# Optimization experiments

Hardware: AMD Instinct MI355X
Metric: run time of the kernel (lower is better)

## Reference

```python
import jax, jax.numpy as jnp
import numpy as np

B, T, N, SD, D, HYP, EMB = 128, 256, 8, 200, 64, 64, 32

def _ln(x, g, b, eps=1e-5):
    mu = jnp.mean(x, -1, keepdims=True)
    v = jnp.mean((x - mu) ** 2, -1, keepdims=True)
    return (x - mu) * jax.lax.rsqrt(v + eps) * g + b

def setup_inputs():
    key = jax.random.key(0)
    ks = iter(jax.random.split(key, 64))
    def p(shape, scale=0.05):
        return (jax.random.normal(next(ks), shape) * scale).astype(jnp.float32)
    n, sd, d, hyp, emb = N, SD, D, HYP, EMB
    return dict(
        qvals=p((B, T, n), 1.0), states=p((B, T, sd), 1.0), hidden_state=p((B, T, n, d), 1.0),
        enc_w1=p((sd, d)), enc_b1=p((d,)), enc_w2=p((d, d)), enc_b2=p((d,)),
        wq=p((d, d)), bq=p((d,)), wk=p((d, d)), bk=p((d,)), wv=p((d, d)), bv=p((d,)),
        wo=p((d, d)), bo=p((d,)),
        ln1_g=jnp.ones((d,), jnp.float32), ln1_b=jnp.zeros((d,), jnp.float32),
        ffn_w1=p((d, d)), ffn_b1=p((d,)), ffn_w2=p((d, d)), ffn_b2=p((d,)),
        ln2_g=jnp.ones((d,), jnp.float32), ln2_b=jnp.zeros((d,), jnp.float32),
        fc2ni_w=p((n, d, n - 1)), fc2ni_b=p((n, n - 1)),
        norm_g=jnp.ones((n - 1,), jnp.float32), norm_b=jnp.zeros((n - 1,), jnp.float32),
        w1a=p((2 * d, hyp)), b1a=p((hyp,)), w1b=p((hyp, n * emb)), b1b=p((n * emb,)),
        hb1w=p((2 * d, emb)), hb1b=p((emb,)),
        w2a=p((2 * d, hyp)), b2a=p((hyp,)), w2b=p((hyp, emb)), b2b=p((emb,)),
        hb2w1=p((2 * d, emb)), hb2b1=p((emb,)), hb2w2=p((emb, 1)), hb2b2=p((1,)))

def reference(qvals, states, hidden_state, enc_w1, enc_b1, enc_w2, enc_b2,
              wq, bq, wk, bk, wv, bv, wo, bo, ln1_g, ln1_b,
              ffn_w1, ffn_b1, ffn_w2, ffn_b2, ln2_g, ln2_b,
              fc2ni_w, fc2ni_b, norm_g, norm_b,
              w1a, b1a, w1b, b1b, hb1w, hb1b,
              w2a, b2a, w2b, b2b, hb2w1, hb2b1, hb2w2, hb2b2):
    sg = jax.lax.stop_gradient
    b, t, n = qvals.shape
    bt = b * t
    d = hidden_state.shape[-1]
    emb = hb1w.shape[1]
    # Encoder_s: relu(fc1) then tanh(fc2(e)+e)
    s = states.reshape(bt, -1)
    e = jax.nn.relu(s @ enc_w1 + enc_b1)
    enc = jnp.tanh(e @ enc_w2 + enc_b2 + e)                       # (bt, 64)
    # concat detached agent hiddens with detached state embedding -> (bt, n+1, 64)
    h = jnp.concatenate([sg(hidden_state.reshape(bt, n, d)), sg(enc)[:, None, :]], axis=1)
    # transformer block (single-head self-attention + FFN, post-LN)
    q = h @ wq + bq; k = h @ wk + bk; v = h @ wv + bv
    att = jax.nn.softmax(jnp.einsum('bid,bjd->bij', q, k) / jnp.sqrt(jnp.float32(d)), axis=-1)
    h2 = _ln(h + (att @ v) @ wo + bo, ln1_g, ln1_b)
    h3 = _ln(h2 + jax.nn.relu(h2 @ ffn_w1 + ffn_b1) @ ffn_w2 + ffn_b2, ln2_g, ln2_b)
    h_trans = h3[:, :n]                                           # (bt, n, 64)
    ens = jnp.concatenate([enc, sg(h_trans).mean(1)], axis=-1)    # (bt, 128)
    # per-agent fc2_Ni -> LayerNorm -> sigmoid, vectorized over agents
    ni = jnp.einsum('xnd,nde->xne', h_trans, fc2ni_w) + fc2ni_b   # (bt, n, n-1)
    ni = jax.nn.sigmoid(_ln(ni, norm_g, norm_b))
    # insert 1.0 at the diagonal (agent i keeps its own q with weight 1)
    rows = jnp.arange(n)[:, None]; cols = jnp.arange(n)[None, :]
    gidx = jnp.clip(cols - (cols > rows).astype(jnp.int32), 0, n - 2)  # (n, n)
    gathered = jnp.take_along_axis(ni, jnp.broadcast_to(gidx, (bt, n, n)), axis=-1)
    nfull = jnp.where(cols == rows, jnp.float32(1.0), gathered)   # (bt, n, n)
    N_nn = nfull.reshape(b, t, n, n)
    q_ni = (qvals[:, :, None, :] * N_nn).sum(-1).reshape(bt, 1, n)
    # hypernetwork mixing (QMIX)
    ens_d = sg(ens)
    w1 = jnp.abs(jax.nn.relu(ens_d @ w1a + b1a) @ w1b + b1b).reshape(bt, n, emb)
    b1 = (ens_d @ hb1w + hb1b).reshape(bt, 1, emb)
    w2 = jnp.abs(jax.nn.relu(ens @ w2a + b2a) @ w2b + b2b).reshape(bt, emb, 1)
    b2 = (jax.nn.relu(ens @ hb2w1 + hb2b1) @ hb2w2 + hb2b2).reshape(bt, 1, 1)
    hidden = jax.nn.elu(q_ni @ w1 + b1)
    y = (hidden @ w2 + b2).reshape(b, t, 1)
    eye_mask = jnp.broadcast_to(jnp.eye(n, dtype=bool), (b, t, n, n))
    return y, N_nn, eye_mask
```

## Files before the change

kernel.cpp:

```cpp
#include <hip/hip_runtime.h>
#include <hip/hip_bf16.h>

typedef __bf16 bf16x8 __attribute__((ext_vector_type(8)));
typedef __bf16 bf16x4 __attribute__((ext_vector_type(4)));
typedef float f32x4 __attribute__((ext_vector_type(4)));

#define ROWSG 32768
#define RB 7
#define NBLK 4682
#define HPAD 72
#define NN_OFF ((size_t)ROWSG)
#define EYE_OFF ((size_t)ROWSG + (size_t)ROWSG*64)

#define OFF_EW1   0
#define OFF_EW2   14336
#define OFF_WQ    18432
#define OFF_WK    22528
#define OFF_WV    26624
#define OFF_WO    30720
#define OFF_F1    34816
#define OFF_F2    38912
#define OFF_W1A   43008
#define OFF_W1B   51200
#define OFF_HB1W  67584
#define OFF_W2A   71680
#define OFF_W2B   79872
#define OFF_HB2W1 81920
#define OFF_NI    86016
#define WS_TOTAL  94208

__device__ __align__(16) __bf16 g_ws[WS_TOTAL];

#define MFMA16(a,b,c) __builtin_amdgcn_mfma_f32_16x16x32_bf16(a,b,c,0,0,0)

struct TP { const float* src[15]; };

__global__ __launch_bounds__(256) void wtrans(TP tp) {
    const int gid = blockIdx.x * 256 + threadIdx.x;
    if (gid >= WS_TOTAL) return;
    if (gid >= OFF_NI) {
        const int loc = gid - OFF_NI;
        const int nmat = loc >> 10, rem = loc & 1023, e = rem >> 6, k = rem & 63;
        float v = (e < 7) ? tp.src[14][nmat * 448 + k * 7 + e] : 0.f;
        g_ws[gid] = (__bf16)v;
        return;
    }
    const int OFFS[14] = {OFF_EW1, OFF_EW2, OFF_WQ, OFF_WK, OFF_WV, OFF_WO, OFF_F1,
                          OFF_F2, OFF_W1A, OFF_W1B, OFF_HB1W, OFF_W2A, OFF_W2B, OFF_HB2W1};
    const int KPS[14]  = {224, 64, 64, 64, 64, 64, 64, 64, 128, 64, 128, 128, 64, 128};
    const int KRS[14]  = {200, 64, 64, 64, 64, 64, 64, 64, 128, 64, 128, 128, 64, 128};
    const int NS[14]   = {64, 64, 64, 64, 64, 64, 64, 64, 64, 256, 32, 64, 32, 32};
    int m = 0;
#pragma unroll
    for (int i = 1; i < 14; ++i) if (gid >= OFFS[i]) m = i;
    const int loc = gid - OFFS[m];
    const int Kp = KPS[m];
    const int n = loc / Kp;
    const int k = loc - n * Kp;
    float v = 0.f;
    if (k < KRS[m]) v = tp.src[m][(size_t)k * NS[m] + n];
    g_ws[gid] = (__bf16)v;
}

struct MainP {
    const float *qvals, *states, *hid, *eb1, *eb2, *bq, *bk, *bv, *bo,
        *l1g, *l1b, *fb1, *fb2, *l2g, *l2b, *niw, *nib, *ng, *nb,
        *b1a, *b1b, *hb1b, *b2a, *b2b, *hb2b1, *hw2, *hb2b2;
    float* out;
};

__device__ __forceinline__ void proj_ln4(const __bf16* A, const __bf16* WT,
                                         const float* bias, const float* g, const float* bb,
                                         __bf16* H, int w, int quad, int l15) {
    const int mt = w;
    f32x4 acc0 = {0,0,0,0}, acc1 = {0,0,0,0}, acc2 = {0,0,0,0}, acc3 = {0,0,0,0};
#pragma unroll
    for (int ks = 0; ks < 2; ++ks) {
        const int kk = ks * 32 + quad * 8;
        const bf16x8 af = *(const bf16x8*)(A + (mt * 16 + l15) * HPAD + kk);
        acc0 = MFMA16(af, *(const bf16x8*)(WT + (size_t)(0 * 16 + l15) * 64 + kk), acc0);
        acc1 = MFMA16(af, *(const bf16x8*)(WT + (size_t)(1 * 16 + l15) * 64 + kk), acc1);
        acc2 = MFMA16(af, *(const bf16x8*)(WT + (size_t)(2 * 16 + l15) * 64 + kk), acc2);
        acc3 = MFMA16(af, *(const bf16x8*)(WT + (size_t)(3 * 16 + l15) * 64 + kk), acc3);
    }
    float v[4][4], g4[4], b4[4];
#pragma unroll
    for (int nt = 0; nt < 4; ++nt) {
        const int col = nt * 16 + l15;
        const float bo = bias[col];
        g4[nt] = g[col]; b4[nt] = bb[col];
        const f32x4 a = (nt == 0) ? acc0 : (nt == 1) ? acc1 : (nt == 2) ? acc2 : acc3;
#pragma unroll
        for (int r = 0; r < 4; ++r)
            v[nt][r] = a[r] + bo + (float)H[(mt * 16 + quad * 4 + r) * HPAD + col];
    }
#pragma unroll
    for (int r = 0; r < 4; ++r) {
        float s  = v[0][r] + v[1][r] + v[2][r] + v[3][r];
        float s2 = v[0][r]*v[0][r] + v[1][r]*v[1][r] + v[2][r]*v[2][r] + v[3][r]*v[3][r];
#pragma unroll
        for (int off = 1; off < 16; off <<= 1) {
            s  += __shfl_xor(s,  off, 64);
            s2 += __shfl_xor(s2, off, 64);
        }
        const float mu  = s * 0.015625f;
        const float var = s2 * 0.015625f - mu * mu;
        const float rs  = rsqrtf(var + 1e-5f);
#pragma unroll
        for (int nt = 0; nt < 4; ++nt)
            H[(mt * 16 + quad * 4 + r) * HPAD + nt * 16 + l15] =
                (__bf16)((v[nt][r] - mu) * rs * g4[nt] + b4[nt]);
    }
}

__global__ __launch_bounds__(256) void mixer_main(MainP p) {
    __shared__ __align__(16) __bf16 Hb[64 * HPAD];
    __shared__ __align__(16) __bf16 Qb[64 * HPAD];
    __shared__ __align__(16) __bf16 Kb[64 * HPAD];
    __shared__ __align__(16) __bf16 EbU[16 * HPAD];
    __shared__ __align__(16) float  attU[7 * 90];
    __shared__ float  qniL[56];

    __bf16* Sb   = Qb;
    __bf16* W1bS = Qb;
    float*  B1f  = (float*)(Qb + 1792);
    float*  W2f  = (float*)(Qb + 2240);
    float*  T3f  = (float*)(Qb + 2688);
    __bf16* Tb2  = Qb + 3136;
    float*  sNiP = (float*)(Qb + 3136);
    __bf16* ensB = Kb;

    const int blk = blockIdx.x;
    const int bt0 = blk * RB;
    const int t = threadIdx.x;
    const int w = t >> 6, lane = t & 63, quad = lane >> 4, l15 = lane & 15;
    const __bf16* ws = g_ws;

#pragma unroll
    for (int it = 0; it < 4; ++it) {
        const int u = it * 256 + t;
        if (u < 896) {
            const int x = u >> 7, rem = u & 127, n = rem >> 4, d4 = (rem & 15) * 4;
            const int bt = bt0 + x;
            const size_t btc = (bt < ROWSG) ? bt : (ROWSG - 1);
            const float4 v4 = *(const float4*)(p.hid + (btc * 512 + n * 64 + d4));
            bf16x4 o; o[0] = (__bf16)v4.x; o[1] = (__bf16)v4.y; o[2] = (__bf16)v4.z; o[3] = (__bf16)v4.w;
            *(bf16x4*)(Hb + (x * 9 + n) * HPAD + d4) = o;
        }
    }
#pragma unroll
    for (int it = 0; it < 2; ++it) {
        const int u = it * 256 + t;
        if (u < 350) {
            const int xr = u / 50, c4 = u - xr * 50;
            const int bt = bt0 + xr;
            const size_t btc = (bt < ROWSG) ? bt : (ROWSG - 1);
            const float4 v4 = *(const float4*)(p.states + btc * 200 + c4 * 4);
            bf16x4 o; o[0] = (__bf16)v4.x; o[1] = (__bf16)v4.y; o[2] = (__bf16)v4.z; o[3] = (__bf16)v4.w;
            *(bf16x4*)(Sb + xr * 224 + c4 * 4) = o;
        }
    }
    if (t < 168) { const int xr = t / 24, c = t - xr * 24; Sb[xr * 224 + 200 + c] = (__bf16)0.0f; }
    __syncthreads();

    float e4[4];
    {
        const int n0 = w * 16;
        const int srow = (l15 < RB) ? l15 : (RB - 1);
        f32x4 acc = {0, 0, 0, 0};
        for (int ks = 0; ks < 7; ++ks) {
            const int kk = ks * 32 + quad * 8;
            const bf16x8 af = *(const bf16x8*)(Sb + srow * 224 + kk);
            const bf16x8 bf = *(const bf16x8*)(ws + OFF_EW1 + (size_t)(n0 + l15) * 224 + kk);
            acc = MFMA16(af, bf, acc);
        }
        const float b1 = p.eb1[n0 + l15];
#pragma unroll
        for (int r = 0; r < 4; ++r) {
            const float ev = fmaxf(acc[r] + b1, 0.f);
            e4[r] = ev;
            EbU[(quad * 4 + r) * HPAD + n0 + l15] = (__bf16)ev;
        }
    }
    __syncthreads();

    {
        const int n0 = w * 16;
        f32x4 acc = {0, 0, 0, 0};
#pragma unroll
        for (int ks = 0; ks < 2; ++ks) {
            const int kk = ks * 32 + quad * 8;
            const bf16x8 af = *(const bf16x8*)(EbU + l15 * HPAD + kk);
            const bf16x8 bf = *(const bf16x8*)(ws + OFF_EW2 + (size_t)(n0 + l15) * 64 + kk);
            acc = MFMA16(af, bf, acc);
        }
        const float b2 = p.eb2[n0 + l15];
#pragma unroll
        for (int r = 0; r < 4; ++r) {
            const int xr = quad * 4 + r;
            if (xr < RB) {
                const float ev = tanhf(acc[r] + e4[r] + b2);
                Hb[(xr * 9 + 8) * HPAD + n0 + l15] = (__bf16)ev;
                EbU[(8 + xr) * HPAD + n0 + l15] = (__bf16)ev;
            }
        }
    }
    __syncthreads();

    for (int it = 0; it < 8; ++it) {
        const int j = w + 4 * it;
        const int mat = j >> 4, r16 = j & 15, mt = r16 >> 2, nt = r16 & 3;
        const __bf16* wt = ws + (mat == 0 ? OFF_WQ : OFF_WK);
        const float* bias = (mat == 0 ? p.bq : p.bk);
        __bf16* dst = (mat == 0 ? Qb : Kb);
        f32x4 acc = {0, 0, 0, 0};
#pragma unroll
        for (int ks = 0; ks < 2; ++ks) {
            const int kk = ks * 32 + quad * 8;
            const bf16x8 af = *(const bf16x8*)(Hb + (mt * 16 + l15) * HPAD + kk);
            const bf16x8 bf = *(const bf16x8*)(wt + (size_t)(nt * 16 + l15) * 64 + kk);
            acc = MFMA16(af, bf, acc);
        }
        const float bv = bias[nt * 16 + l15];
#pragma unroll
        for (int r = 0; r < 4; ++r)
            dst[(mt * 16 + quad * 4 + r) * HPAD + nt * 16 + l15] = (__bf16)(acc[r] + bv);
    }
    __syncthreads();

    for (int xi = 0; xi < 2; ++xi) {
        const int x = w * 2 + xi;
        if (x >= RB) continue;
        {
            const int arow = (x * 9 + ((l15 < 9) ? l15 : 8)) * HPAD;
            f32x4 acc = {0, 0, 0, 0};
#pragma unroll
            for (int ks = 0; ks < 2; ++ks) {
                const int kk = ks * 32 + quad * 8;
                const bf16x8 qa = *(const bf16x8*)(Qb + arow + kk);
                const bf16x8 kb = *(const bf16x8*)(Kb + arow + kk);
                acc = MFMA16(qa, kb, acc);
            }
#pragma unroll
            for (int r = 0; r < 4; ++r) {
                const int i = quad * 4 + r;
                float s = (l15 < 9) ? acc[r] * 0.125f : -3.0e38f;
                float m = s;
#pragma unroll
                for (int off = 1; off < 16; off <<= 1) m = fmaxf(m, __shfl_xor(m, off, 64));
                float e = (l15 < 9) ? __expf(s - m) : 0.f;
                float sum = e;
#pragma unroll
                for (int off = 1; off < 16; off <<= 1) sum += __shfl_xor(sum, off, 64);
                const float pv = e / sum;
                if (i < 9 && l15 < 9) attU[x * 90 + i * 10 + l15] = pv;
            }
        }
        {
            float vreg[9];
#pragma unroll
            for (int jj = 0; jj < 9; ++jj) vreg[jj] = (float)Hb[(x * 9 + jj) * HPAD + lane];
#pragma unroll
            for (int i = 0; i < 9; ++i) {
                const float* ar = attU + x * 90 + i * 10;
                const float2 a0 = *(const float2*)(ar);
                const float2 a1 = *(const float2*)(ar + 2);
                const float2 a2 = *(const float2*)(ar + 4);
                const float2 a3 = *(const float2*)(ar + 6);
                const float a8 = ar[8];
                const float a = a0.x * vreg[0] + a0.y * vreg[1] + a1.x * vreg[2] + a1.y * vreg[3]
                              + a2.x * vreg[4] + a2.y * vreg[5] + a3.x * vreg[6] + a3.y * vreg[7]
                              + a8 * vreg[8];
                Kb[(x * 9 + i) * HPAD + lane] = (__bf16)a;
            }
        }
    }
    __syncthreads();

    for (int it = 0; it < 4; ++it) {
        const int j = w + 4 * it;
        const int mt = j >> 2, nt = j & 3;
        f32x4 acc = {0, 0, 0, 0};
#pragma unroll
        for (int ks = 0; ks < 2; ++ks) {
            const int kk = ks * 32 + quad * 8;
            const bf16x8 af = *(const bf16x8*)(Kb + (mt * 16 + l15) * HPAD + kk);
            const bf16x8 bf = *(const bf16x8*)(ws + OFF_WV + (size_t)(nt * 16 + l15) * 64 + kk);
            acc = MFMA16(af, bf, acc);
        }
        const float bv = p.bv[nt * 16 + l15];
#pragma unroll
        for (int r = 0; r < 4; ++r)
            Qb[(mt * 16 + quad * 4 + r) * HPAD + nt * 16 + l15] = (__bf16)(acc[r] + bv);
    }
    __syncthreads();

    proj_ln4(Qb, ws + OFF_WO, p.bo, p.l1g, p.l1b, Hb, w, quad, l15);
    __syncthreads();

    for (int it = 0; it < 4; ++it) {
        const int j = w + 4 * it;
        const int mt = j >> 2, nt = j & 3;
        f32x4 acc = {0, 0, 0, 0};
#pragma unroll
        for (int ks = 0; ks < 2; ++ks) {
            const int kk = ks * 32 + quad * 8;
            const bf16x8 af = *(const bf16x8*)(Hb + (mt * 16 + l15) * HPAD + kk);
            const bf16x8 bf = *(const bf16x8*)(ws + OFF_F1 + (size_t)(nt * 16 + l15) * 64 + kk);
            acc = MFMA16(af, bf, acc);
        }
        const float fb = p.fb1[nt * 16 + l15];
#pragma unroll
        for (int r = 0; r < 4; ++r)
            Kb[(mt * 16 + quad * 4 + r) * HPAD + nt * 16 + l15] = (__bf16)fmaxf(acc[r] + fb, 0.f);
    }
    __syncthreads();

    proj_ln4(Kb, ws + OFF_F2, p.fb2, p.l2g, p.l2b, Hb, w, quad, l15);
    __syncthreads();

    {
#pragma unroll
        for (int it = 0; it < 2; ++it) {
            const int u = it * 256 + t;
            if (u < RB * 64) {
                const int x = u >> 6, col = u & 63;
                float s = 0.f;
#pragma unroll
                for (int i = 0; i < 8; ++i) s += (float)Hb[(x * 9 + i) * HPAD + col];
                ensB[x * 136 + 64 + col] = (__bf16)(s * 0.125f);
                ensB[x * 136 + col] = EbU[(8 + x) * HPAD + col];
            }
        }
    }
    for (int jn = 0; jn < 2; ++jn) {
        const int n = w * 2 + jn;
        const int l15c = (l15 < RB) ? l15 : (RB - 1);
        f32x4 acc = {0, 0, 0, 0};
#pragma unroll
        for (int ks = 0; ks < 2; ++ks) {
            const int kk = ks * 32 + quad * 8;
            const bf16x8 af = *(const bf16x8*)(Hb + (l15c * 9 + n) * HPAD + kk);
            const bf16x8 bf = *(const bf16x8*)(ws + OFF_NI + n * 1024 + (size_t)l15 * 64 + kk);
            acc = MFMA16(af, bf, acc);
        }
#pragma unroll
        for (int r = 0; r < 4; ++r) {
            const int x = quad * 4 + r;
            const float av = (l15 < 7) ? (acc[r] + p.nib[n * 7 + l15]) : 0.f;
            float s1 = av;
            s1 += __shfl_xor(s1, 1, 64); s1 += __shfl_xor(s1, 2, 64);
            s1 += __shfl_xor(s1, 4, 64); s1 += __shfl_xor(s1, 8, 64);
            const float mu = s1 * (1.f / 7.f);
            float d0 = (l15 < 7) ? (av - mu) : 0.f;
            float s2 = d0 * d0;
            s2 += __shfl_xor(s2, 1, 64); s2 += __shfl_xor(s2, 2, 64);
            s2 += __shfl_xor(s2, 4, 64); s2 += __shfl_xor(s2, 8, 64);
            const float rs = rsqrtf(s2 * (1.f / 7.f) + 1e-5f);
            if (x < RB && l15 < 7) {
                const float vv = (av - mu) * rs * p.ng[l15] + p.nb[l15];
                sNiP[(x * 8 + n) * 7 + l15] = 1.f / (1.f + __expf(-vv));
            }
        }
    }
    __syncthreads();

    {
        float* Nf = attU;
        if (t < RB * 16) {
            const int x = t >> 4, c4 = (t & 15) * 4;
            const int i = c4 >> 3;
            float4 nv, ev;
            float* nvp = &nv.x; float* evp = &ev.x;
#pragma unroll
            for (int k = 0; k < 4; ++k) {
                const int rem = c4 + k, jj = rem & 7;
                const float nf = (i == jj) ? 1.f : sNiP[(x * 8 + i) * 7 + jj - (jj > i ? 1 : 0)];
                nvp[k] = nf;
                evp[k] = (i == jj) ? 1.f : 0.f;
            }
            const int bt = bt0 + x;
            if (bt < ROWSG) {
                *(float4*)(p.out + NN_OFF + (size_t)bt * 64 + c4) = nv;
                *(float4*)(p.out + EYE_OFF + (size_t)bt * 64 + c4) = ev;
            }
            *(float4*)(Nf + x * 64 + c4) = nv;
        }
    }
    __syncthreads();

    if (t < RB * 32) {
        const float* Nf = attU;
        const int pr = t >> 2, q4 = t & 3;
        const int x = pr >> 3, i = pr & 7;
        const int j0 = q4 * 2;
        const int bt = bt0 + x;
        const size_t btc = (bt < ROWSG) ? bt : (ROWSG - 1);
        const float2 qv = *(const float2*)(p.qvals + btc * 8 + j0);
        const float2 nf2 = *(const float2*)(Nf + x * 64 + i * 8 + j0);
        float s = qv.x * nf2.x + qv.y * nf2.y;
        s += __shfl_xor(s, 1, 64);
        s += __shfl_xor(s, 2, 64);
        if (q4 == 0) qniL[x * 8 + i] = s;
    }
    {
        const int n0 = w * 16;
#pragma unroll
        for (int m2 = 0; m2 < 2; ++m2) {
            const __bf16* wt = ws + (m2 == 0 ? OFF_W1A : OFF_W2A);
            const float* bias = m2 == 0 ? p.b1a : p.b2a;
            __bf16* dst = m2 == 0 ? EbU : Tb2;
            f32x4 acc = {0, 0, 0, 0};
#pragma unroll
            for (int ks = 0; ks < 4; ++ks) {
                const int kk = ks * 32 + quad * 8;
                const bf16x8 af = *(const bf16x8*)(ensB + l15 * 136 + kk);
                const bf16x8 bf = *(const bf16x8*)(wt + (size_t)(n0 + l15) * 128 + kk);
                acc = MFMA16(af, bf, acc);
            }
            const float bb = bias[n0 + l15];
#pragma unroll
            for (int r = 0; r < 4; ++r)
                dst[(quad * 4 + r) * HPAD + n0 + l15] = (__bf16)fmaxf(acc[r] + bb, 0.f);
        }
    }
    __syncthreads();

    for (int it = 0; it < 6; ++it) {
        const int j = w + 4 * it;
        if (j >= 22) continue;
        int mode, n0, Kp, ksteps, aStride;
        const __bf16 *A, *WT; const float* bias;
        if (j < 16)      { mode = 0; n0 = j * 16;        A = EbU;  aStride = HPAD; WT = ws + OFF_W1B;   bias = p.b1b;  Kp = 64;  ksteps = 2; }
        else if (j < 18) { mode = 1; n0 = (j - 16) * 16; A = ensB; aStride = 136;  WT = ws + OFF_HB1W;  bias = p.hb1b; Kp = 128; ksteps = 4; }
        else if (j < 20) { mode = 2; n0 = (j - 18) * 16; A = Tb2;  aStride = HPAD; WT = ws + OFF_W2B;   bias = p.b2b;  Kp = 64;  ksteps = 2; }
        else             { mode = 3; n0 = (j - 20) * 16; A = ensB; aStride = 136;  WT = ws + OFF_HB2W1; bias = p.hb2b1;Kp = 128; ksteps = 4; }
        f32x4 acc = {0, 0, 0, 0};
        for (int ks = 0; ks < ksteps; ++ks) {
            const int kk = ks * 32 + quad * 8;
            const bf16x8 af = *(const bf16x8*)(A + l15 * aStride + kk);
            const bf16x8 bf = *(const bf16x8*)(WT + (size_t)(n0 + l15) * Kp + kk);
            acc = MFMA16(af, bf, acc);
        }
        const float bb = bias[n0 + l15];
#pragma unroll
        for (int r = 0; r < 4; ++r) {
            const int xr = quad * 4 + r;
            if (xr < RB) {
                const float val = acc[r] + bb;
                if (mode == 0)      W1bS[xr * 256 + n0 + l15] = (__bf16)fabsf(val);
                else if (mode == 1) B1f[xr * 32 + n0 + l15] = val;
                else if (mode == 2) W2f[xr * 32 + n0 + l15] = fabsf(val);
                else                T3f[xr * 32 + n0 + l15] = fmaxf(val, 0.f);
            }
        }
    }
    __syncthreads();

    if (t < RB * 16) {
        const int x = t >> 4, sub = t & 15;
        float pp = 0.f, pb = 0.f;
#pragma unroll
        for (int h2i = 0; h2i < 2; ++h2i) {
            const int e = sub + h2i * 16;
            float a = B1f[x * 32 + e];
#pragma unroll
            for (int i = 0; i < 8; ++i) a += qniL[x * 8 + i] * (float)W1bS[x * 256 + i * 32 + e];
            const float hid = a > 0.f ? a : (__expf(a) - 1.f);
            pp += hid * W2f[x * 32 + e];
            pb += T3f[x * 32 + e] * p.hw2[e];
        }
#pragma unroll
        for (int off = 1; off < 16; off <<= 1) {
            pp += __shfl_xor(pp, off, 64);
            pb += __shfl_xor(pb, off, 64);
        }
        const int bt = bt0 + x;
        if (sub == 0 && bt < ROWSG) p.out[bt] = pp + pb + p.hb2b2[0];
    }
}

extern "C" void kernel_launch(void* const* d_in, const int* in_sizes, int n_in,
                              void* d_out, int out_size, void* d_ws, size_t ws_size,
                              hipStream_t stream) {
    TP tp;
    tp.src[0]  = (const float*)d_in[3];
    tp.src[1]  = (const float*)d_in[5];
    tp.src[2]  = (const float*)d_in[7];
    tp.src[3]  = (const float*)d_in[9];
    tp.src[4]  = (const float*)d_in[11];
    tp.src[5]  = (const float*)d_in[13];
    tp.src[6]  = (const float*)d_in[17];
    tp.src[7]  = (const float*)d_in[19];
    tp.src[8]  = (const float*)d_in[27];
    tp.src[9]  = (const float*)d_in[29];
    tp.src[10] = (const float*)d_in[31];
    tp.src[11] = (const float*)d_in[33];
    tp.src[12] = (const float*)d_in[35];
    tp.src[13] = (const float*)d_in[37];
    tp.src[14] = (const float*)d_in[23];
    wtrans<<<(WS_TOTAL + 255) / 256, 256, 0, stream>>>(tp);

    MainP p;
    p.qvals = (const float*)d_in[0];
    p.states = (const float*)d_in[1];
    p.hid = (const float*)d_in[2];
    p.eb1 = (const float*)d_in[4];
    p.eb2 = (const float*)d_in[6];
    p.bq = (const float*)d_in[8];
    p.bk = (const float*)d_in[10];
    p.bv = (const float*)d_in[12];
    p.bo = (const float*)d_in[14];
    p.l1g = (const float*)d_in[15];
    p.l1b = (const float*)d_in[16];
    p.fb1 = (const float*)d_in[18];
    p.fb2 = (const float*)d_in[20];
    p.l2g = (const float*)d_in[21];
    p.l2b = (const float*)d_in[22];
    p.niw = (const float*)d_in[23];
    p.nib = (const float*)d_in[24];
    p.ng = (const float*)d_in[25];
    p.nb = (const float*)d_in[26];
    p.b1a = (const float*)d_in[28];
    p.b1b = (const float*)d_in[30];
    p.hb1b = (const float*)d_in[32];
    p.b2a = (const float*)d_in[34];
    p.b2b = (const float*)d_in[36];
    p.hb2b1 = (const float*)d_in[38];
    p.hw2 = (const float*)d_in[39];
    p.hb2b2 = (const float*)d_in[40];
    p.out = (float*)d_out;

    mixer_main<<<NBLK, 256, 0, stream>>>(p);
}
```

Measured before the change: 381.8 us.

## Fold Wq·Wk^T into a single bilinear form and drop the K projection buffer

Attention scores are rewritten algebraically as H·(Wq Wk^T)·H^T plus rank-one bias terms (H·Wq·bk, H·Wk·bq, bq·bk). The combined matrix is precomputed in the weight-prep kernel, so the main kernel needs one projection instead of separate Q and K projections. This also frees the Kb shared buffer and cuts LDS use. The V projection is restructured into a single tile per wave. The cost is extra precompute work in the prep kernel, plus a precision change because the fused matrix is rounded to bf16.

```diff
diff --git a/kernel.cpp b/kernel.cpp
--- a/kernel.cpp
+++ b/kernel.cpp
@@ -15,7 +15,7 @@
 #define OFF_EW1   0
 #define OFF_EW2   14336
 #define OFF_WQ    18432
-#define OFF_WK    22528
+#define OFF_QKU   22528
 #define OFF_WV    26624
 #define OFF_WO    30720
 #define OFF_F1    34816
@@ -30,14 +30,39 @@
 #define WS_TOTAL  94208
 
 __device__ __align__(16) __bf16 g_ws[WS_TOTAL];
+__device__ float g_qkc;
 
 #define MFMA16(a,b,c) __builtin_amdgcn_mfma_f32_16x16x32_bf16(a,b,c,0,0,0)
 
-struct TP { const float* src[15]; };
+struct TP { const float* src[17]; };
 
 __global__ __launch_bounds__(256) void wtrans(TP tp) {
     const int gid = blockIdx.x * 256 + threadIdx.x;
     if (gid >= WS_TOTAL) return;
+    if (gid == 0) {
+        float c = 0.f;
+        for (int e = 0; e < 64; ++e) c += tp.src[15][e] * tp.src[16][e];
+        g_qkc = c;
+    }
+    if (gid >= OFF_WQ && gid < OFF_WQ + 4096) {
+        const int loc = gid - OFF_WQ;
+        const int n = loc >> 6, d = loc & 63;
+        const float* wq = tp.src[2];
+        const float* wk = tp.src[3];
+        float v = 0.f;
+        for (int e = 0; e < 64; ++e) v += wq[d * 64 + e] * wk[n * 64 + e];
+        g_ws[gid] = (__bf16)v;
+        return;
+    }
+    if (gid >= OFF_QKU && gid < OFF_QKU + 4096) {
+        const int loc = gid - OFF_QKU;
+        const int rrow = loc >> 6, d = loc & 63;
+        float v = 0.f;
+        if (rrow == 0) { for (int e = 0; e < 64; ++e) v += tp.src[2][d * 64 + e] * tp.src[16][e]; }
+        else if (rrow == 1) { for (int e = 0; e < 64; ++e) v += tp.src[3][d * 64 + e] * tp.src[15][e]; }
+        g_ws[gid] = (__bf16)v;
+        return;
+    }
     if (gid >= OFF_NI) {
         const int loc = gid - OFF_NI;
         const int nmat = loc >> 10, rem = loc & 1023, e = rem >> 6, k = rem & 63;
@@ -45,20 +70,21 @@
         g_ws[gid] = (__bf16)v;
         return;
     }
-    const int OFFS[14] = {OFF_EW1, OFF_EW2, OFF_WQ, OFF_WK, OFF_WV, OFF_WO, OFF_F1,
+    const int OFFS[12] = {OFF_EW1, OFF_EW2, OFF_WV, OFF_WO, OFF_F1,
                           OFF_F2, OFF_W1A, OFF_W1B, OFF_HB1W, OFF_W2A, OFF_W2B, OFF_HB2W1};
-    const int KPS[14]  = {224, 64, 64, 64, 64, 64, 64, 64, 128, 64, 128, 128, 64, 128};
-    const int KRS[14]  = {200, 64, 64, 64, 64, 64, 64, 64, 128, 64, 128, 128, 64, 128};
-    const int NS[14]   = {64, 64, 64, 64, 64, 64, 64, 64, 64, 256, 32, 64, 32, 32};
+    const int SRCI[12] = {0, 1, 4, 5, 6, 7, 8, 9, 10, 11, 12, 13};
+    const int KPS[12]  = {224, 64, 64, 64, 64, 64, 128, 64, 128, 128, 64, 128};
+    const int KRS[12]  = {200, 64, 64, 64, 64, 64, 128, 64, 128, 128, 64, 128};
+    const int NS[12]   = {64, 64, 64, 64, 64, 64, 64, 256, 32, 64, 32, 32};
     int m = 0;
 #pragma unroll
-    for (int i = 1; i < 14; ++i) if (gid >= OFFS[i]) m = i;
+    for (int i = 1; i < 12; ++i) if (gid >= OFFS[i]) m = i;
     const int loc = gid - OFFS[m];
     const int Kp = KPS[m];
     const int n = loc / Kp;
     const int k = loc - n * Kp;
     float v = 0.f;
-    if (k < KRS[m]) v = tp.src[m][(size_t)k * NS[m] + n];
+    if (k < KRS[m]) v = tp.src[SRCI[m]][(size_t)k * NS[m] + n];
     g_ws[gid] = (__bf16)v;
 }
 
@@ -116,10 +142,10 @@
 __global__ __launch_bounds__(256) void mixer_main(MainP p) {
     __shared__ __align__(16) __bf16 Hb[64 * HPAD];
     __shared__ __align__(16) __bf16 Qb[64 * HPAD];
-    __shared__ __align__(16) __bf16 Kb[64 * HPAD];
     __shared__ __align__(16) __bf16 EbU[16 * HPAD];
     __shared__ __align__(16) float  attU[7 * 90];
     __shared__ float  qniL[56];
+    __shared__ __align__(16) __bf16 ensB[7 * 136];
 
     __bf16* Sb   = Qb;
     __bf16* W1bS = Qb;
@@ -128,7 +154,6 @@
     float*  T3f  = (float*)(Qb + 2688);
     __bf16* Tb2  = Qb + 3136;
     float*  sNiP = (float*)(Qb + 3136);
-    __bf16* ensB = Kb;
 
     const int blk = blockIdx.x;
     const int bt0 = blk * RB;
@@ -207,24 +232,30 @@
     }
     __syncthreads();
 
-    for (int it = 0; it < 8; ++it) {
+    for (int it = 0; it < 5; ++it) {
         const int j = w + 4 * it;
-        const int mat = j >> 4, r16 = j & 15, mt = r16 >> 2, nt = r16 & 3;
-        const __bf16* wt = ws + (mat == 0 ? OFF_WQ : OFF_WK);
-        const float* bias = (mat == 0 ? p.bq : p.bk);
-        __bf16* dst = (mat == 0 ? Qb : Kb);
+        const int uv = (j >= 16);
+        const int mt = uv ? (j - 16) : (j >> 2);
+        const int nt = uv ? 4 : (j & 3);
+        const __bf16* wt = uv ? (ws + OFF_QKU + (size_t)l15 * 64)
+                              : (ws + OFF_WQ + (size_t)(nt * 16 + l15) * 64);
         f32x4 acc = {0, 0, 0, 0};
 #pragma unroll
         for (int ks = 0; ks < 2; ++ks) {
             const int kk = ks * 32 + quad * 8;
             const bf16x8 af = *(const bf16x8*)(Hb + (mt * 16 + l15) * HPAD + kk);
-            const bf16x8 bf = *(const bf16x8*)(wt + (size_t)(nt * 16 + l15) * 64 + kk);
+            const bf16x8 bf = *(const bf16x8*)(wt + kk);
             acc = MFMA16(af, bf, acc);
         }
-        const float bv = bias[nt * 16 + l15];
-#pragma unroll
-        for (int r = 0; r < 4; ++r)
-            dst[(mt * 16 + quad * 4 + r) * HPAD + nt * 16 + l15] = (__bf16)(acc[r] + bv);
+        if (!uv) {
+#pragma unroll
+            for (int r = 0; r < 4; ++r)
+                Qb[(mt * 16 + quad * 4 + r) * HPAD + nt * 16 + l15] = (__bf16)acc[r];
+        } else if (l15 < 8) {
+#pragma unroll
+            for (int r = 0; r < 4; ++r)
+                Qb[(mt * 16 + quad * 4 + r) * HPAD + 64 + l15] = (__bf16)acc[r];
+        }
     }
     __syncthreads();
 
@@ -232,19 +263,24 @@
         const int x = w * 2 + xi;
         if (x >= RB) continue;
         {
-            const int arow = (x * 9 + ((l15 < 9) ? l15 : 8)) * HPAD;
+            const int rowc = x * 9 + ((l15 < 9) ? l15 : 8);
+            const int arow = rowc * HPAD;
             f32x4 acc = {0, 0, 0, 0};
 #pragma unroll
             for (int ks = 0; ks < 2; ++ks) {
                 const int kk = ks * 32 + quad * 8;
                 const bf16x8 qa = *(const bf16x8*)(Qb + arow + kk);
-                const bf16x8 kb = *(const bf16x8*)(Kb + arow + kk);
-                acc = MFMA16(qa, kb, acc);
-            }
+                const bf16x8 hb = *(const bf16x8*)(Hb + arow + kk);
+                acc = MFMA16(qa, hb, acc);
+            }
+            const float vj = (float)Qb[arow + 65];
+            const float cc = g_qkc;
 #pragma unroll
             for (int r = 0; r < 4; ++r) {
                 const int i = quad * 4 + r;
-                float s = (l15 < 9) ? acc[r] * 0.125f : -3.0e38f;
+                const int ic = (i < 9) ? i : 8;
+                const float ui = (float)Qb[(x * 9 + ic) * HPAD + 64];
+                float s = (l15 < 9) ? (acc[r] + ui + vj + cc) * 0.125f : -3.0e38f;
                 float m = s;
 #pragma unroll
                 for (int off = 1; off < 16; off <<= 1) m = fmaxf(m, __shfl_xor(m, off, 64));
@@ -271,10 +307,33 @@
                 const float a = a0.x * vreg[0] + a0.y * vreg[1] + a1.x * vreg[2] + a1.y * vreg[3]
                               + a2.x * vreg[4] + a2.y * vreg[5] + a3.x * vreg[6] + a3.y * vreg[7]
                               + a8 * vreg[8];
-                Kb[(x * 9 + i) * HPAD + lane] = (__bf16)a;
-            }
-        }
-    }
+                Qb[(x * 9 + i) * HPAD + lane] = (__bf16)a;
+            }
+        }
+    }
+    __syncthreads();
+
+    {
+        f32x4 acc[4] = {{0,0,0,0},{0,0,0,0},{0,0,0,0},{0,0,0,0}};
+#pragma unroll
+        for (int ks = 0; ks < 2; ++ks) {
+            const int kk = ks * 32 + quad * 8;
+            const bf16x8 af = *(const bf16x8*)(Qb + (w * 16 + l15) * HPAD + kk);
+#pragma unroll
+            for (int nt = 0; nt < 4; ++nt)
+                acc[nt] = MFMA16(af, *(const bf16x8*)(ws + OFF_WV + (size_t)(nt * 16 + l15) * 64 + kk), acc[nt]);
+        }
+#pragma unroll
+        for (int nt = 0; nt < 4; ++nt) {
+            const float bv = p.bv[nt * 16 + l15];
+#pragma unroll
+            for (int r = 0; r < 4; ++r)
+                Qb[(w * 16 + quad * 4 + r) * HPAD + nt * 16 + l15] = (__bf16)(acc[nt][r] + bv);
+        }
+    }
+    __syncthreads();
+
+    proj_ln4(Qb, ws + OFF_WO, p.bo, p.l1g, p.l1b, Hb, w, quad, l15);
     __syncthreads();
 
     for (int it = 0; it < 4; ++it) {
@@ -284,27 +343,6 @@
 #pragma unroll
         for (int ks = 0; ks < 2; ++ks) {
             const int kk = ks * 32 + quad * 8;
-            const bf16x8 af = *(const bf16x8*)(Kb + (mt * 16 + l15) * HPAD + kk);
-            const bf16x8 bf = *(const bf16x8*)(ws + OFF_WV + (size_t)(nt * 16 + l15) * 64 + kk);
-            acc = MFMA16(af, bf, acc);
-        }
-        const float bv = p.bv[nt * 16 + l15];
-#pragma unroll
-        for (int r = 0; r < 4; ++r)
-            Qb[(mt * 16 + quad * 4 + r) * HPAD + nt * 16 + l15] = (__bf16)(acc[r] + bv);
-    }
-    __syncthreads();
-
-    proj_ln4(Qb, ws + OFF_WO, p.bo, p.l1g, p.l1b, Hb, w, quad, l15);
-    __syncthreads();
-
-    for (int it = 0; it < 4; ++it) {
-        const int j = w + 4 * it;
-        const int mt = j >> 2, nt = j & 3;
-        f32x4 acc = {0, 0, 0, 0};
-#pragma unroll
-        for (int ks = 0; ks < 2; ++ks) {
-            const int kk = ks * 32 + quad * 8;
             const bf16x8 af = *(const bf16x8*)(Hb + (mt * 16 + l15) * HPAD + kk);
             const bf16x8 bf = *(const bf16x8*)(ws + OFF_F1 + (size_t)(nt * 16 + l15) * 64 + kk);
             acc = MFMA16(af, bf, acc);
@@ -312,11 +350,11 @@
         const float fb = p.fb1[nt * 16 + l15];
 #pragma unroll
         for (int r = 0; r < 4; ++r)
-            Kb[(mt * 16 + quad * 4 + r) * HPAD + nt * 16 + l15] = (__bf16)fmaxf(acc[r] + fb, 0.f);
-    }
-    __syncthreads();
-
-    proj_ln4(Kb, ws + OFF_F2, p.fb2, p.l2g, p.l2b, Hb, w, quad, l15);
+            Qb[(mt * 16 + quad * 4 + r) * HPAD + nt * 16 + l15] = (__bf16)fmaxf(acc[r] + fb, 0.f);
+    }
+    __syncthreads();
+
+    proj_ln4(Qb, ws + OFF_F2, p.fb2, p.l2g, p.l2b, Hb, w, quad, l15);
     __syncthreads();
 
     {
@@ -499,6 +537,8 @@
     tp.src[12] = (const float*)d_in[35];
     tp.src[13] = (const float*)d_in[37];
     tp.src[14] = (const float*)d_in[23];
+    tp.src[15] = (const float*)d_in[8];
+    tp.src[16] = (const float*)d_in[10];
     wtrans<<<(WS_TOTAL + 255) / 256, 256, 0, stream>>>(tp);
 
     MainP p;
```

New measurement: 389.1 us. No clear change (+1.9%).
